# Performance work log

Hardware: AMD Instinct MI355X
Metric: run time of the kernel (lower is better)

Reference implementation:

```python
import jax, jax.numpy as jnp
import numpy as np
from jax import lax

GAMMA = 1.0

def _conv(x, w, b, stride, pad):
    y = lax.conv_general_dilated(x, w, (stride, stride), [(pad, pad), (pad, pad)],
                                 dimension_numbers=('NCHW', 'OIHW', 'NCHW'))
    return y + b[None, :, None, None]

def _maxpool2s1(x):
    return lax.reduce_window(x, -jnp.inf, lax.max, (1, 1, 2, 2), (1, 1, 1, 1), 'VALID')

def setup_inputs() -> dict:
    key = jax.random.key(0)
    ks = jax.random.split(key, 13)
    d = {}
    d['x'] = jax.random.normal(ks[0], (128, 3, 250, 250), dtype=jnp.float32)
    d['conv1_w'] = jax.random.normal(ks[1], (6, 3, 5, 5), dtype=jnp.float32) / np.sqrt(3 * 25)
    d['conv1_b'] = jax.random.normal(ks[2], (6,), dtype=jnp.float32) * 0.01
    d['conv2_w'] = jax.random.normal(ks[3], (15, 6, 3, 3), dtype=jnp.float32) / np.sqrt(6 * 9)
    d['conv2_b'] = jax.random.normal(ks[4], (15,), dtype=jnp.float32) * 0.01
    d['fc1_w'] = jax.random.normal(ks[5], (120, 55815), dtype=jnp.float32) / np.sqrt(55815.0)
    d['fc1_b'] = jax.random.normal(ks[6], (120,), dtype=jnp.float32) * 0.01
    d['fc2_w'] = jax.random.normal(ks[7], (84, 120), dtype=jnp.float32) / np.sqrt(120.0)
    d['fc2_b'] = jax.random.normal(ks[8], (84,), dtype=jnp.float32) * 0.01
    d['fc3_w'] = jax.random.normal(ks[9], (1, 84), dtype=jnp.float32) / np.sqrt(84.0)
    d['fc3_b'] = jax.random.normal(ks[10], (1,), dtype=jnp.float32) * 0.01
    d['support'] = jax.random.normal(ks[11], (10, 1), dtype=jnp.float32)
    return d

def reference(x, conv1_w, conv1_b, conv2_w, conv2_b, fc1_w, fc1_b, fc2_w, fc2_b, fc3_w, fc3_b, support):
    h = jax.nn.relu(_conv(x, conv1_w, conv1_b, 2, 1))   # [B,6,124,124]
    h = _maxpool2s1(h)                                   # [B,6,123,123] (dropout = identity in eval)
    h = jax.nn.relu(_conv(h, conv2_w, conv2_b, 2, 1))    # [B,15,62,62]
    h = _maxpool2s1(h)                                   # [B,15,61,61]
    h = h.reshape(h.shape[0], -1)                        # [B,55815]
    h = jax.nn.relu(h @ fc1_w.T + fc1_b)
    h = jax.nn.relu(h @ fc2_w.T + fc2_b)
    h = h @ fc3_w.T + fc3_b                              # [B,1]
    # fused RBF kernel vs support set: k[i,j] = exp(-gamma*(x_i - s_j)^2)
    diff = h - support[:, 0][None, :]                    # [B,10]
    k = jnp.exp(-GAMMA * diff * diff)
    h = k.mean(axis=1, keepdims=True)                    # [B,1]
    probs = jax.nn.sigmoid(h)
    return jnp.concatenate((probs, 1.0 - probs), axis=-1)  # [B,2]
```

## Files before the change

kernel.cpp:

```cpp
#include <hip/hip_runtime.h>
#include <math.h>


#define BATCH 128

#define C1_ST 150
#define C1_TOT (37 * 133)
__global__ __launch_bounds__(256) void conv1_pool_kernel(
    const float* __restrict__ x, const float* __restrict__ w,
    const float* __restrict__ bias, float* __restrict__ out) {
  const int b = blockIdx.z;
  const int P0 = blockIdx.x * 64;
  const int R0 = blockIdx.y * 16;
  const int tid = threadIdx.x;
  const int t = tid >> 4;
  const int s = tid & 15;

  __shared__ float lds[37 * C1_ST];

  float acc0[5][6], acc1[5][6];
#pragma unroll
  for (int oc = 0; oc < 6; oc++) {
    float bv = bias[oc];
#pragma unroll
    for (int dc = 0; dc < 5; dc++) { acc0[dc][oc] = bv; acc1[dc][oc] = bv; }
  }

  const int ihb = 2 * R0 - 1, iwb = 2 * P0 - 1;

#pragma unroll 1
  for (int ci = 0; ci < 3; ci++) {
    __syncthreads();
    const float* src = x + (size_t)(b * 3 + ci) * 62500;
#pragma unroll 1
    for (int base = tid; base < C1_TOT; base += 2048) {
      float vv[8];
#pragma unroll
      for (int k = 0; k < 8; k++) {
        int i = base + (k << 8);
        int lr = i / 133, il = i - lr * 133;
        int ih = ihb + lr, iw = iwb + il;
        bool ok = (i < C1_TOT) && ((unsigned)ih < 250u) && ((unsigned)iw < 250u);
        vv[k] = ok ? src[ih * 250 + iw] : 0.f;
      }
#pragma unroll
      for (int k = 0; k < 8; k++) {
        int i = base + (k << 8);
        if (i < C1_TOT) {
          int lr = i / 133, il = i - lr * 133;
          lds[lr * C1_ST + il + (il >> 3)] = vv[k];
        }
      }
    }
    __syncthreads();

#pragma unroll 1
    for (int ir = 0; ir < 7; ir++) {
      const float* rp = &lds[(2 * t + ir) * C1_ST + 9 * s];
      float v[13];
#pragma unroll
      for (int j = 0; j < 13; j++) v[j] = rp[j + (j >> 3)];

      if (ir < 5) {
#pragma unroll
        for (int oc = 0; oc < 6; oc++) {
          const float* wr = w + ((oc * 3 + ci) * 5 + ir) * 5;
          float w0 = wr[0], w1 = wr[1], w2 = wr[2], w3 = wr[3], w4 = wr[4];
#pragma unroll
          for (int dc = 0; dc < 5; dc++) {
            float a = acc0[dc][oc];
            a += w0 * v[2 * dc + 0];
            a += w1 * v[2 * dc + 1];
            a += w2 * v[2 * dc + 2];
            a += w3 * v[2 * dc + 3];
            a += w4 * v[2 * dc + 4];
            acc0[dc][oc] = a;
          }
        }
      }
      if (ir >= 2) {
#pragma unroll
        for (int oc = 0; oc < 6; oc++) {
          const float* wr = w + ((oc * 3 + ci) * 5 + (ir - 2)) * 5;
          float w0 = wr[0], w1 = wr[1], w2 = wr[2], w3 = wr[3], w4 = wr[4];
#pragma unroll
          for (int dc = 0; dc < 5; dc++) {
            float a = acc1[dc][oc];
            a += w0 * v[2 * dc + 0];
            a += w1 * v[2 * dc + 1];
            a += w2 * v[2 * dc + 2];
            a += w3 * v[2 * dc + 3];
            a += w4 * v[2 * dc + 4];
            acc1[dc][oc] = a;
          }
        }
      }
    }
  }

  const int r = R0 + t;
  if (r < 123) {
#pragma unroll
    for (int oc = 0; oc < 6; oc++) {
      float* orow = out + ((size_t)(b * 6 + oc) * 123 + r) * 123;
#pragma unroll
      for (int i = 0; i < 4; i++) {
        int c = P0 + 4 * s + i;
        if (c < 123) {
          float m = fmaxf(fmaxf(acc0[i][oc], acc0[i + 1][oc]),
                          fmaxf(acc1[i][oc], acc1[i + 1][oc]));
          orow[c] = fmaxf(m, 0.f);
        }
      }
    }
  }
}

#define C2_ST 84
#define C2_TOT (35 * 67)
__global__ __launch_bounds__(256) void conv2_pool_kernel(
    const float* __restrict__ in, const float* __restrict__ w,
    const float* __restrict__ bias, float* __restrict__ out) {
  const int b = blockIdx.z;
  const int P0 = blockIdx.x * 32;
  const int R0 = blockIdx.y * 16;
  const int tid = threadIdx.x;
  const int t = tid >> 4;
  const int s = tid & 15;

  __shared__ float lds[35 * C2_ST];

  float acc0[3][15], acc1[3][15];
#pragma unroll
  for (int k = 0; k < 15; k++) {
    float bv = bias[k];
#pragma unroll
    for (int dc = 0; dc < 3; dc++) { acc0[dc][k] = bv; acc1[dc][k] = bv; }
  }

  const int ihb = 2 * R0 - 1, iwb = 2 * P0 - 1;

#pragma unroll 1
  for (int ci = 0; ci < 6; ci++) {
    __syncthreads();
    const float* src = in + (size_t)(b * 6 + ci) * 15129;
#pragma unroll 1
    for (int base = tid; base < C2_TOT; base += 2048) {
      float vv[8];
#pragma unroll
      for (int k = 0; k < 8; k++) {
        int i = base + (k << 8);
        int lr = i / 67, il = i - lr * 67;
        int ih = ihb + lr, iw = iwb + il;
        bool ok = (i < C2_TOT) && ((unsigned)ih < 123u) && ((unsigned)iw < 123u);
        vv[k] = ok ? src[ih * 123 + iw] : 0.f;
      }
#pragma unroll
      for (int k = 0; k < 8; k++) {
        int i = base + (k << 8);
        if (i < C2_TOT) {
          int lr = i / 67, il = i - lr * 67;
          lds[lr * C2_ST + il + (il >> 2)] = vv[k];
        }
      }
    }
    __syncthreads();

#pragma unroll 1
    for (int ir = 0; ir < 5; ir++) {
      const float* rp = &lds[(2 * t + ir) * C2_ST + 5 * s];
      float v[7];
#pragma unroll
      for (int j = 0; j < 7; j++) v[j] = rp[j + (j >> 2)];

      if (ir < 3) {
#pragma unroll
        for (int k = 0; k < 15; k++) {
          const float* wr = w + ((k * 6 + ci) * 3 + ir) * 3;
          float w0 = wr[0], w1 = wr[1], w2 = wr[2];
#pragma unroll
          for (int dc = 0; dc < 3; dc++) {
            float a = acc0[dc][k];
            a += w0 * v[2 * dc + 0];
            a += w1 * v[2 * dc + 1];
            a += w2 * v[2 * dc + 2];
            acc0[dc][k] = a;
          }
        }
      }
      if (ir >= 2) {
#pragma unroll
        for (int k = 0; k < 15; k++) {
          const float* wr = w + ((k * 6 + ci) * 3 + (ir - 2)) * 3;
          float w0 = wr[0], w1 = wr[1], w2 = wr[2];
#pragma unroll
          for (int dc = 0; dc < 3; dc++) {
            float a = acc1[dc][k];
            a += w0 * v[2 * dc + 0];
            a += w1 * v[2 * dc + 1];
            a += w2 * v[2 * dc + 2];
            acc1[dc][k] = a;
          }
        }
      }
    }
  }

  const int r = R0 + t;
  if (r < 61) {
#pragma unroll
    for (int k = 0; k < 15; k++) {
      float* orow = out + ((size_t)(b * 15 + k) * 61 + r) * 61;
#pragma unroll
      for (int i = 0; i < 2; i++) {
        int c = P0 + 2 * s + i;
        if (c < 61) {
          float m = fmaxf(fmaxf(acc0[i][k], acc0[i + 1][k]),
                          fmaxf(acc1[i][k], acc1[i + 1][k]));
          orow[c] = fmaxf(m, 0.f);
        }
      }
    }
  }
}

#define KTOT 55815
#define NPART 512
#define KCHUNK 112
__global__ __launch_bounds__(256) void fc1_splitk_kernel(
    const float* __restrict__ act, const float* __restrict__ w,
    float* __restrict__ partial) {
  const int kbase = blockIdx.x * KCHUNK;
  const int tid = threadIdx.x;
  const int tx = tid % 16, ty = tid / 16;
  __shared__ float ldsA[8 * 132];
  __shared__ float ldsB[8 * 132];
  float acc[8][8];
#pragma unroll
  for (int i = 0; i < 8; i++)
#pragma unroll
    for (int j = 0; j < 8; j++) acc[i][j] = 0.f;

  for (int s8 = 0; s8 < KCHUNK / 8; s8++) {
    int kofs = kbase + s8 * 8;
    __syncthreads();
    for (int i = tid; i < 1024; i += 256) {
      int m = i >> 3, kk = i & 7;
      int k = kofs + kk;
      ldsA[kk * 132 + m] = (k < KTOT) ? act[m * KTOT + k] : 0.f;
    }
    for (int i = tid; i < 960; i += 256) {
      int n = i >> 3, kk = i & 7;
      int k = kofs + kk;
      ldsB[kk * 132 + n] = (k < KTOT) ? w[n * KTOT + k] : 0.f;
    }
    __syncthreads();
#pragma unroll
    for (int kk = 0; kk < 8; kk++) {
      float4 a0 = *(const float4*)&ldsA[kk * 132 + ty * 8];
      float4 a1 = *(const float4*)&ldsA[kk * 132 + ty * 8 + 4];
      float4 b0 = *(const float4*)&ldsB[kk * 132 + tx * 8];
      float4 b1 = *(const float4*)&ldsB[kk * 132 + tx * 8 + 4];
      float av[8] = {a0.x, a0.y, a0.z, a0.w, a1.x, a1.y, a1.z, a1.w};
      float bv[8] = {b0.x, b0.y, b0.z, b0.w, b1.x, b1.y, b1.z, b1.w};
#pragma unroll
      for (int i = 0; i < 8; i++)
#pragma unroll
        for (int j = 0; j < 8; j++) acc[i][j] += av[i] * bv[j];
    }
  }

  float* dst = partial + (size_t)blockIdx.x * 15360;
#pragma unroll
  for (int i = 0; i < 8; i++) {
    int row = ty * 8 + i;
#pragma unroll
    for (int j = 0; j < 8; j++) {
      int col = tx * 8 + j;
      if (col < 120) dst[row * 120 + col] = acc[i][j];
    }
  }
}

__global__ __launch_bounds__(64) void fc1_reduce1_kernel(
    const float* __restrict__ partial, float* __restrict__ partial2) {
  int idx = blockIdx.x * 64 + threadIdx.x;
  int g = blockIdx.y;
  const float* p = partial + (size_t)g * 64 * 15360 + idx;
  float s = 0.f;
#pragma unroll 8
  for (int q = 0; q < 64; q++) s += p[(size_t)q * 15360];
  partial2[(size_t)g * 15360 + idx] = s;
}

__global__ __launch_bounds__(64) void fc1_reduce2_kernel(
    const float* __restrict__ partial2, const float* __restrict__ bias,
    float* __restrict__ h1) {
  int idx = blockIdx.x * 64 + threadIdx.x;
  float s = 0.f;
#pragma unroll
  for (int g = 0; g < 8; g++) s += partial2[(size_t)g * 15360 + idx];
  h1[idx] = fmaxf(s + bias[idx % 120], 0.f);
}

__global__ __launch_bounds__(128) void head_kernel(
    const float* __restrict__ h1, const float* __restrict__ fc2_w,
    const float* __restrict__ fc2_b, const float* __restrict__ fc3_w,
    const float* __restrict__ fc3_b, const float* __restrict__ support,
    float* __restrict__ out) {
  int b = blockIdx.x, t = threadIdx.x;
  __shared__ float hrow[120];
  __shared__ float s2[84];
  if (t < 120) hrow[t] = h1[b * 120 + t];
  __syncthreads();
  if (t < 84) {
    float d = fc2_b[t];
    for (int k = 0; k < 120; k++) d += fc2_w[t * 120 + k] * hrow[k];
    s2[t] = fmaxf(d, 0.f);
  }
  __syncthreads();
  if (t == 0) {
    float h = fc3_b[0];
    for (int j = 0; j < 84; j++) h += fc3_w[j] * s2[j];
    float ks = 0.f;
    for (int j = 0; j < 10; j++) {
      float diff = h - support[j];
      ks += expf(-diff * diff);
    }
    ks *= 0.1f;
    float p = 1.f / (1.f + expf(-ks));
    out[b * 2] = p;
    out[b * 2 + 1] = 1.f - p;
  }
}

extern "C" void kernel_launch(void* const* d_in, const int* in_sizes, int n_in,
                              void* d_out, int out_size, void* d_ws, size_t ws_size,
                              hipStream_t stream) {
  const float* x   = (const float*)d_in[0];
  const float* c1w = (const float*)d_in[1];
  const float* c1b = (const float*)d_in[2];
  const float* c2w = (const float*)d_in[3];
  const float* c2b = (const float*)d_in[4];
  const float* f1w = (const float*)d_in[5];
  const float* f1b = (const float*)d_in[6];
  const float* f2w = (const float*)d_in[7];
  const float* f2b = (const float*)d_in[8];
  const float* f3w = (const float*)d_in[9];
  const float* f3b = (const float*)d_in[10];
  const float* sup = (const float*)d_in[11];
  float* out = (float*)d_out;

  char* ws = (char*)d_ws;
  float* pool1 = (float*)ws;
  float* act   = (float*)(ws + 46476288);
  float* part  = (float*)ws;
  float* h1    = (float*)(ws + 33000000);
  float* part2 = (float*)(ws + 34000000);

  conv1_pool_kernel<<<dim3(2, 8, BATCH), 256, 0, stream>>>(x, c1w, c1b, pool1);
  conv2_pool_kernel<<<dim3(2, 4, BATCH), 256, 0, stream>>>(pool1, c2w, c2b, act);
  fc1_splitk_kernel<<<NPART, 256, 0, stream>>>(act, f1w, part);
  fc1_reduce1_kernel<<<dim3(240, 8), 64, 0, stream>>>(part, part2);
  fc1_reduce2_kernel<<<240, 64, 0, stream>>>(part2, f1b, h1);
  head_kernel<<<BATCH, 128, 0, stream>>>(h1, f2w, f2b, f3w, f3b, sup, out);
}
```

Measured before the change: 382.0 us.

## Compute two pooled rows per thread in conv1 and add occupancy launch bounds

Each conv1 thread now produces two pooled output rows and keeps three conv-row accumulators, so each loaded input row is reused across more output rows. This lets the block shrink to 128 threads while covering the same tile. Launch-bound occupancy hints are also added to the conv1, conv2 and fc1 kernels. The extra accumulators raise register pressure, and the occupancy hints may force spills.

Result: slower. 475.3 us (+24.4%).

```diff
diff --git a/kernel.cpp b/kernel.cpp
--- a/kernel.cpp
+++ b/kernel.cpp
@@ -6,24 +6,26 @@
 
 #define C1_ST 150
 #define C1_TOT (37 * 133)
-__global__ __launch_bounds__(256) void conv1_pool_kernel(
+__global__ __launch_bounds__(128, 4) void conv1_pool_kernel(
     const float* __restrict__ x, const float* __restrict__ w,
     const float* __restrict__ bias, float* __restrict__ out) {
   const int b = blockIdx.z;
   const int P0 = blockIdx.x * 64;
   const int R0 = blockIdx.y * 16;
   const int tid = threadIdx.x;
-  const int t = tid >> 4;
+  const int tg = tid >> 4;
   const int s = tid & 15;
 
   __shared__ float lds[37 * C1_ST];
 
-  float acc0[5][6], acc1[5][6];
+  float acc0[5][6], acc1[5][6], acc2[5][6];
 #pragma unroll
   for (int oc = 0; oc < 6; oc++) {
     float bv = bias[oc];
 #pragma unroll
-    for (int dc = 0; dc < 5; dc++) { acc0[dc][oc] = bv; acc1[dc][oc] = bv; }
+    for (int dc = 0; dc < 5; dc++) {
+      acc0[dc][oc] = bv; acc1[dc][oc] = bv; acc2[dc][oc] = bv;
+    }
   }
 
   const int ihb = 2 * R0 - 1, iwb = 2 * P0 - 1;
@@ -33,11 +35,11 @@
     __syncthreads();
     const float* src = x + (size_t)(b * 3 + ci) * 62500;
 #pragma unroll 1
-    for (int base = tid; base < C1_TOT; base += 2048) {
+    for (int base = tid; base < C1_TOT; base += 1024) {
       float vv[8];
 #pragma unroll
       for (int k = 0; k < 8; k++) {
-        int i = base + (k << 8);
+        int i = base + (k << 7);
         int lr = i / 133, il = i - lr * 133;
         int ih = ihb + lr, iw = iwb + il;
         bool ok = (i < C1_TOT) && ((unsigned)ih < 250u) && ((unsigned)iw < 250u);
@@ -45,7 +47,7 @@
       }
 #pragma unroll
       for (int k = 0; k < 8; k++) {
-        int i = base + (k << 8);
+        int i = base + (k << 7);
         if (i < C1_TOT) {
           int lr = i / 133, il = i - lr * 133;
           lds[lr * C1_ST + il + (il >> 3)] = vv[k];
@@ -55,13 +57,13 @@
     __syncthreads();
 
 #pragma unroll 1
-    for (int ir = 0; ir < 7; ir++) {
-      const float* rp = &lds[(2 * t + ir) * C1_ST + 9 * s];
+    for (int ir = 0; ir < 9; ir++) {
+      const float* rp = &lds[(4 * tg + ir) * C1_ST + 9 * s];
       float v[13];
 #pragma unroll
       for (int j = 0; j < 13; j++) v[j] = rp[j + (j >> 3)];
 
-      if (ir < 5) {
+      if (ir <= 4) {
 #pragma unroll
         for (int oc = 0; oc < 6; oc++) {
           const float* wr = w + ((oc * 3 + ci) * 5 + ir) * 5;
@@ -78,7 +80,7 @@
           }
         }
       }
-      if (ir >= 2) {
+      if (ir >= 2 && ir <= 6) {
 #pragma unroll
         for (int oc = 0; oc < 6; oc++) {
           const float* wr = w + ((oc * 3 + ci) * 5 + (ir - 2)) * 5;
@@ -95,14 +97,31 @@
           }
         }
       }
-    }
-  }
-
-  const int r = R0 + t;
-  if (r < 123) {
+      if (ir >= 4) {
+#pragma unroll
+        for (int oc = 0; oc < 6; oc++) {
+          const float* wr = w + ((oc * 3 + ci) * 5 + (ir - 4)) * 5;
+          float w0 = wr[0], w1 = wr[1], w2 = wr[2], w3 = wr[3], w4 = wr[4];
+#pragma unroll
+          for (int dc = 0; dc < 5; dc++) {
+            float a = acc2[dc][oc];
+            a += w0 * v[2 * dc + 0];
+            a += w1 * v[2 * dc + 1];
+            a += w2 * v[2 * dc + 2];
+            a += w3 * v[2 * dc + 3];
+            a += w4 * v[2 * dc + 4];
+            acc2[dc][oc] = a;
+          }
+        }
+      }
+    }
+  }
+
+  const int pr = R0 + 2 * tg;
+  if (pr < 123) {
 #pragma unroll
     for (int oc = 0; oc < 6; oc++) {
-      float* orow = out + ((size_t)(b * 6 + oc) * 123 + r) * 123;
+      float* orow = out + ((size_t)(b * 6 + oc) * 123 + pr) * 123;
 #pragma unroll
       for (int i = 0; i < 4; i++) {
         int c = P0 + 4 * s + i;
@@ -114,11 +133,26 @@
       }
     }
   }
+  if (pr + 1 < 123) {
+#pragma unroll
+    for (int oc = 0; oc < 6; oc++) {
+      float* orow = out + ((size_t)(b * 6 + oc) * 123 + pr + 1) * 123;
+#pragma unroll
+      for (int i = 0; i < 4; i++) {
+        int c = P0 + 4 * s + i;
+        if (c < 123) {
+          float m = fmaxf(fmaxf(acc1[i][oc], acc1[i + 1][oc]),
+                          fmaxf(acc2[i][oc], acc2[i + 1][oc]));
+          orow[c] = fmaxf(m, 0.f);
+        }
+      }
+    }
+  }
 }
 
 #define C2_ST 84
 #define C2_TOT (35 * 67)
-__global__ __launch_bounds__(256) void conv2_pool_kernel(
+__global__ __launch_bounds__(256, 3) void conv2_pool_kernel(
     const float* __restrict__ in, const float* __restrict__ w,
     const float* __restrict__ bias, float* __restrict__ out) {
   const int b = blockIdx.z;
@@ -227,7 +261,7 @@
 #define KTOT 55815
 #define NPART 512
 #define KCHUNK 112
-__global__ __launch_bounds__(256) void fc1_splitk_kernel(
+__global__ __launch_bounds__(256, 4) void fc1_splitk_kernel(
     const float* __restrict__ act, const float* __restrict__ w,
     float* __restrict__ partial) {
   const int kbase = blockIdx.x * KCHUNK;
@@ -358,7 +392,7 @@
   float* h1    = (float*)(ws + 33000000);
   float* part2 = (float*)(ws + 34000000);
 
-  conv1_pool_kernel<<<dim3(2, 8, BATCH), 256, 0, stream>>>(x, c1w, c1b, pool1);
+  conv1_pool_kernel<<<dim3(2, 8, BATCH), 128, 0, stream>>>(x, c1w, c1b, pool1);
   conv2_pool_kernel<<<dim3(2, 4, BATCH), 256, 0, stream>>>(pool1, c2w, c2b, act);
   fc1_splitk_kernel<<<NPART, 256, 0, stream>>>(act, f1w, part);
   fc1_reduce1_kernel<<<dim3(240, 8), 64, 0, stream>>>(part, part2);
```
